# Performance work log

Measured on AMD Instinct MI355X. Metric: run time of the kernel, lower is better.

## Reference

```python
import jax, jax.numpy as jnp
import numpy as np
import math

B, S, D, H = 8, 1024, 256, 8
HD = D // H  # head size = 32


def setup_inputs() -> dict:
    key = jax.random.key(0)
    ks = jax.random.split(key, 12)
    inp = {
        "query": jax.random.normal(ks[0], (B, S, D), jnp.float32),
        "key": jax.random.normal(ks[1], (B, S, D), jnp.float32),
        "value": jax.random.normal(ks[2], (B, S, D), jnp.float32),
        "rel": jax.random.uniform(ks[3], (B, S, S), jnp.float32),
        "timestamp": jax.random.normal(ks[4], (B, S, S), jnp.float32),
        "l1": jax.random.uniform(ks[5], (1,), jnp.float32),
        "l2": jax.random.uniform(ks[6], (1,), jnp.float32),
        # projection weights (nn.Linear: y = x @ W.T + b)
        "Wq": jax.random.normal(ks[7], (D, D), jnp.float32) / math.sqrt(D),
        "bq": jnp.zeros((D,), jnp.float32),
        "Wk": jax.random.normal(ks[8], (D, D), jnp.float32) / math.sqrt(D),
        "bk": jnp.zeros((D,), jnp.float32),
        "Wv": jax.random.normal(ks[9], (D, D), jnp.float32) / math.sqrt(D),
        "bv": jnp.zeros((D,), jnp.float32),
    }
    return inp


def reference(query, key, value, rel, timestamp, l1, l2, Wq, bq, Wk, bk, Wv, bv):
    b, s, d = query.shape
    h, hd = H, HD

    def proj(x, W, bias):
        # [b,s,d] -> [b,h,s,hd]
        return (x @ W.T + bias).reshape(b, s, h, hd).transpose(0, 2, 1, 3)

    q = proj(query, Wq, bq)
    k = proj(key, Wk, bk)
    v = proj(value, Wv, bv)

    # causal future mask: True above the diagonal (future positions)
    mask = jnp.triu(jnp.ones((s, s), dtype=bool), k=1)[None, None]  # [1,1,s,s]

    # relation attention: rel * mask, zeros -> -10000, softmax
    relm = rel[:, None] * mask.astype(rel.dtype)  # broadcast over heads [b,1->h,s,s]
    rel_attn = jax.nn.softmax(jnp.where(relm == 0, jnp.float32(-10000.0), relm), axis=-1)

    # scaled dot-product scores with causal mask
    scores = jnp.einsum('bhqd,bhkd->bhqk', q, k) / math.sqrt(hd)
    scores = jnp.where(mask, jnp.float32(-1e9), scores)
    prob_attn = jax.nn.softmax(scores, axis=-1)

    # time-decay attention: exp(-|t|), masked to -inf (use -1e30 for grad safety)
    ts = jnp.where(mask, jnp.float32(-1e30), jnp.exp(-jnp.abs(timestamp[:, None])))
    time_attn = jax.nn.softmax(ts, axis=-1)

    # blend (time_include=True, qrelation_include=True)
    prob = (1.0 - l2) * prob_attn + l2 * time_attn
    prob = (1.0 - l1) * prob + l1 * rel_attn

    out = jnp.einsum('bhqk,bhkd->bhqd', prob, v)
    out = out.transpose(0, 2, 1, 3).reshape(b, s, d)
    return out
```

## Files before the change

### kernel.cpp

```cpp
#include <hip/hip_runtime.h>
#include <math.h>

constexpr int B = 8, S = 1024, D = 256, H = 8, HD = 32;

typedef __attribute__((ext_vector_type(8))) short bf16x8;
typedef __attribute__((ext_vector_type(16))) float f32x16;
typedef __attribute__((ext_vector_type(2)))  int  int2v;

__device__ __forceinline__ uint cvtpk(float a, float b) {
    uint r;
    asm("v_cvt_pk_bf16_f32 %0, %1, %2" : "=v"(r) : "v"(a), "v"(b));
    return r;
}
__device__ __forceinline__ float xswap32f(float v, int hi) {
    int2v t = __builtin_amdgcn_permlane32_swap(__float_as_int(v), __float_as_int(v), false, false);
    return __int_as_float(hi ? t[0] : t[1]);
}

__global__ __launch_bounds__(512, 4) void proj_mfma(
    const float* __restrict__ query, const float* __restrict__ key_,
    const float* __restrict__ value,
    const float* __restrict__ Wq, const float* __restrict__ Wk,
    const float* __restrict__ Wv,
    const float* __restrict__ bq, const float* __restrict__ bk,
    const float* __restrict__ bv, float qscale,
    ushort* __restrict__ qbuf, ushort* __restrict__ kbuf,
    ushort* __restrict__ vtbuf, float* __restrict__ cpart)
{
    __shared__ ushort xf[8192];
    __shared__ float bias_lds[256];

    const int m = blockIdx.y;
    const int tid = threadIdx.x;
    const int w = tid >> 6, lane = tid & 63;
    const int l31 = lane & 31, hi = lane >> 5;
    const int h = w;

    const float* xsrc = (m == 0) ? query : (m == 1) ? key_ : value;
    const float* Wsrc = (m == 0) ? Wq : (m == 1) ? Wk : Wv;
    const float* bsrc = (m == 0) ? bq : (m == 1) ? bk : bv;
    ushort* yb = (m == 0) ? qbuf : (m == 1) ? kbuf : vtbuf;
    const float wscale = (m == 0) ? qscale : 1.0f;

    if (tid < 256) bias_lds[tid] = bsrc[tid] * wscale;

    bf16x8 wf[16];
    {
        const float* wrow = Wsrc + ((size_t)(h * 32 + l31)) * 256 + hi * 8;
        #pragma unroll
        for (int kc = 0; kc < 16; ++kc) {
            float4 a = *(const float4*)(wrow + kc * 16);
            float4 b = *(const float4*)(wrow + kc * 16 + 4);
            uint4 p;
            p.x = cvtpk(a.x * wscale, a.y * wscale);
            p.y = cvtpk(a.z * wscale, a.w * wscale);
            p.z = cvtpk(b.x * wscale, b.y * wscale);
            p.w = cvtpk(b.z * wscale, b.w * wscale);
            wf[kc] = __builtin_bit_cast(bf16x8, p);
        }
    }

    const int sst = tid & 31, skc = tid >> 5;
    float cpacc = 0.f;

    for (int it = 0; it < 2; ++it) {
        const int stile = blockIdx.x * 2 + it;
        const int b_ = stile >> 5, t32 = stile & 31;

        __syncthreads();
        {
            const float* xrow = xsrc + ((size_t)(stile * 32 + sst)) * 256 + skc * 16;
            float4 a0 = *(const float4*)(xrow + 0);
            float4 a1 = *(const float4*)(xrow + 4);
            float4 a2 = *(const float4*)(xrow + 8);
            float4 a3 = *(const float4*)(xrow + 12);
            uint2 w01 = { cvtpk(a0.x, a0.y), cvtpk(a0.z, a0.w) };
            uint2 w23 = { cvtpk(a1.x, a1.y), cvtpk(a1.z, a1.w) };
            uint2 w45 = { cvtpk(a2.x, a2.y), cvtpk(a2.z, a2.w) };
            uint2 w67 = { cvtpk(a3.x, a3.y), cvtpk(a3.z, a3.w) };
            ushort* base = xf + skc * 512 + sst * 4;
            *(uint2*)(base +   0) = w01;
            *(uint2*)(base + 128) = w23;
            *(uint2*)(base + 256) = w45;
            *(uint2*)(base + 384) = w67;
        }
        __syncthreads();

        f32x16 acc;
        #pragma unroll
        for (int r = 0; r < 16; ++r) acc[r] = 0.f;
        #pragma unroll
        for (int kc = 0; kc < 16; ++kc) {
            const ushort* rb = xf + kc * 512 + hi * 256 + l31 * 4;
            uint2 lo = *(const uint2*)rb;
            uint2 hj = *(const uint2*)(rb + 128);
            uint4 xw = { lo.x, lo.y, hj.x, hj.y };
            bf16x8 xfrag = __builtin_bit_cast(bf16x8, xw);
            if (m < 2)
                acc = __builtin_amdgcn_mfma_f32_32x32x16_bf16(wf[kc], xfrag, acc, 0, 0, 0);
            else
                acc = __builtin_amdgcn_mfma_f32_32x32x16_bf16(xfrag, wf[kc], acc, 0, 0, 0);
        }

        if (m < 2) {
            #pragma unroll
            for (int r = 0; r < 16; ++r)
                acc[r] += bias_lds[h * 32 + (r & 3) + 8 * (r >> 2) + 4 * hi];
        } else {
            const float bl = bias_lds[h * 32 + l31];
            #pragma unroll
            for (int r = 0; r < 16; ++r) acc[r] += bl;
            float cp = 0.f;
            #pragma unroll
            for (int r = 0; r < 16; ++r) cp += acc[r];
            cp += __shfl_xor(cp, 32);
            cpacc += cp;
        }

        uint wa0 = cvtpk(acc[0], acc[1]),   wa1 = cvtpk(acc[2], acc[3]);
        uint wb0 = cvtpk(acc[4], acc[5]),   wb1 = cvtpk(acc[6], acc[7]);
        uint wa2 = cvtpk(acc[8], acc[9]),   wa3 = cvtpk(acc[10], acc[11]);
        uint wb2 = cvtpk(acc[12], acc[13]), wb3 = cvtpk(acc[14], acc[15]);
        int2v s0 = __builtin_amdgcn_permlane32_swap((int)wa0, (int)wb0, false, false);
        int2v s1 = __builtin_amdgcn_permlane32_swap((int)wa1, (int)wb1, false, false);
        int2v s2 = __builtin_amdgcn_permlane32_swap((int)wa2, (int)wb2, false, false);
        int2v s3 = __builtin_amdgcn_permlane32_swap((int)wa3, (int)wb3, false, false);
        uint4 p0 = { (uint)s0[0], (uint)s1[0], (uint)s0[1], (uint)s1[1] };
        uint4 p1 = { (uint)s2[0], (uint)s3[0], (uint)s2[1], (uint)s3[1] };
        ushort* dst = yb + (((size_t)b_ * H + h) * 32 + t32) * 1024 + hi * 256 + l31 * 8;
        *(uint4*)dst = p0;
        *(uint4*)(dst + 512) = p1;
    }
    if (m == 2 && hi == 0)
        cpart[blockIdx.x * D + h * 32 + l31] = cpacc;
}

__global__ __launch_bounds__(512, 2) void timerel_mfma(
    const float* __restrict__ ts, const float* __restrict__ rel,
    const ushort* __restrict__ vtb, const float* __restrict__ cpart,
    const float* __restrict__ l1p, const float* __restrict__ l2p,
    float* __restrict__ out)
{
    __shared__ ushort wlds[66 * 512];
    __shared__ float rsum[2][8][32];
    __shared__ float normt[32], normr[32], nuni[32];

    const int b  = blockIdx.y;
    const int i0 = blockIdx.x * 32;
    const int ksd = i0 >> 4;
    const int w = threadIdx.x >> 6, lane = threadIdx.x & 63;
    const int l31 = lane & 31, hi = lane >> 5;
    const int hi8 = hi * 8;
    const int i = i0 + l31;

    const float* tsrow  = ts  + ((size_t)b * S + i) * S + hi8;
    const float* relrow = rel + ((size_t)b * S + i) * S + hi8;

    float st = 0.f, sr = 0.f;
    const int ks0 = w * 8;
    #pragma unroll
    for (int kk = 0; kk < 8; ++kk) {
        const int ks = ks0 + kk;
        const int js = ks * 16;
        ushort* slotT = wlds + ks * 512 + hi * 256 + l31 * 4;
        if (ks < ksd) {
            float tv[8];
            *(float4*)&tv[0] = *(const float4*)(tsrow + js);
            *(float4*)&tv[4] = *(const float4*)(tsrow + js + 4);
            uint wp[4];
            #pragma unroll
            for (int q = 0; q < 4; ++q) {
                float w0 = __expf(__expf(-fabsf(tv[2 * q])));
                float w1 = __expf(__expf(-fabsf(tv[2 * q + 1])));
                st += w0 + w1;
                wp[q] = cvtpk(w0, w1);
            }
            uint2 v0; v0.x = wp[0]; v0.y = wp[1];
            uint2 v1; v1.x = wp[2]; v1.y = wp[3];
            *(uint2*)slotT         = v0;
            *(uint2*)(slotT + 128) = v1;
        } else if (ks > ksd + 1) {
            float rv[8];
            *(float4*)&rv[0] = *(const float4*)(relrow + js);
            *(float4*)&rv[4] = *(const float4*)(relrow + js + 4);
            uint wp[4];
            #pragma unroll
            for (int q = 0; q < 4; ++q) {
                float r0 = rv[2 * q], r1 = rv[2 * q + 1];
                float w0 = (r0 != 0.f) ? __expf(r0) : 0.f;
                float w1 = (r1 != 0.f) ? __expf(r1) : 0.f;
                sr += w0 + w1;
                wp[q] = cvtpk(w0, w1);
            }
            uint2 v0; v0.x = wp[0]; v0.y = wp[1];
            uint2 v1; v1.x = wp[2]; v1.y = wp[3];
            *(uint2*)slotT         = v0;
            *(uint2*)(slotT + 128) = v1;
        } else {
            float tv[8], rv[8];
            *(float4*)&tv[0] = *(const float4*)(tsrow + js);
            *(float4*)&tv[4] = *(const float4*)(tsrow + js + 4);
            *(float4*)&rv[0] = *(const float4*)(relrow + js);
            *(float4*)&rv[4] = *(const float4*)(relrow + js + 4);
            uint wpT[4], wpR[4];
            #pragma unroll
            for (int q = 0; q < 4; ++q) {
                const int j0 = js + hi8 + 2 * q;
                const bool p0 = (j0     <= i), p1 = (j0 + 1 <= i);
                float t0 = __expf(__expf(-fabsf(tv[2 * q])));
                float t1 = __expf(__expf(-fabsf(tv[2 * q + 1])));
                float r0 = (rv[2 * q]     != 0.f) ? __expf(rv[2 * q])     : 0.f;
                float r1 = (rv[2 * q + 1] != 0.f) ? __expf(rv[2 * q + 1]) : 0.f;
                float wT0 = p0 ? t0 : 0.f, wT1 = p1 ? t1 : 0.f;
                float wR0 = p0 ? 0.f : r0, wR1 = p1 ? 0.f : r1;
                st += wT0 + wT1; sr += wR0 + wR1;
                wpT[q] = cvtpk(wT0, wT1);
                wpR[q] = cvtpk(wR0, wR1);
            }
            uint2 t0v; t0v.x = wpT[0]; t0v.y = wpT[1];
            uint2 t1v; t1v.x = wpT[2]; t1v.y = wpT[3];
            *(uint2*)slotT         = t0v;
            *(uint2*)(slotT + 128) = t1v;
            ushort* slotR = wlds + (64 + (ks - ksd)) * 512 + hi * 256 + l31 * 4;
            uint2 r0v; r0v.x = wpR[0]; r0v.y = wpR[1];
            uint2 r1v; r1v.x = wpR[2]; r1v.y = wpR[3];
            *(uint2*)slotR         = r0v;
            *(uint2*)(slotR + 128) = r1v;
        }
    }

    st += __shfl_xor(st, 32);
    sr += __shfl_xor(sr, 32);
    if (hi == 0) { rsum[0][w][l31] = st; rsum[1][w][l31] = sr; }
    __syncthreads();

    if (threadIdx.x < 32) {
        const int r = threadIdx.x;
        float stt = 0.f, srt = 0.f;
        #pragma unroll
        for (int q = 0; q < 8; ++q) { stt += rsum[0][q][r]; srt += rsum[1][q][r]; }
        const float l1 = l1p[0], l2 = l2p[0];
        normt[r] = (1.f - l1) * l2 / stt;
        normr[r] = (srt > 0.5f) ? (l1 / srt) : 0.f;
        nuni[r]  = (srt > 0.5f) ? 0.f : (l1 / (float)S);
    }
    __syncthreads();

    const ushort* vtbase = vtb + ((size_t)b * 8 + w) * 32768 + hi * 256 + l31 * 8;
    f32x16 accT, accR;
    #pragma unroll
    for (int r = 0; r < 16; ++r) { accT[r] = 0.f; accR[r] = 0.f; }

    #define MSTEP(SLOT, VCH, ACC) do { \
        const ushort* rb = wlds + (SLOT) * 512 + hi * 256 + l31 * 4; \
        uint2 lo = *(const uint2*)rb; \
        uint2 hj = *(const uint2*)(rb + 128); \
        uint4 aw = { lo.x, lo.y, hj.x, hj.y }; \
        bf16x8 afrag = __builtin_bit_cast(bf16x8, aw); \
        bf16x8 vf = *(const bf16x8*)(vtbase + (size_t)(VCH) * 512); \
        ACC = __builtin_amdgcn_mfma_f32_32x32x16_bf16(afrag, vf, ACC, 0, 0, 0); \
    } while (0)

    const int nT = ksd + 2;
    #pragma unroll 4
    for (int ks = 0; ks < nT; ++ks) MSTEP(ks, ks, accT);
    MSTEP(64, ksd,     accR);
    MSTEP(65, ksd + 1, accR);
    #pragma unroll 4
    for (int ks = nT; ks < 64; ++ks) MSTEP(ks, ks, accR);
    #undef MSTEP

    const int d = w * 32 + l31;
    float cv = 0.f;
    if (i0 == S - 32) {
        #pragma unroll
        for (int p_ = 0; p_ < 16; ++p_)
            cv += cpart[(b * 16 + p_) * D + d];
    }
    float* obase = out + ((size_t)b * S + i0) * D + d;
    #pragma unroll
    for (int r = 0; r < 16; ++r) {
        const int row = (r & 3) + 8 * (r >> 2) + 4 * hi;
        obase[(size_t)row * D] =
            accT[r] * normt[row] + accR[r] * normr[row] + nuni[row] * cv;
    }
}

#define LOADKV(K0, K1, V0, V1, KT) do { \
    const ushort* kp_ = kbase + (size_t)(KT) * 1024; \
    const ushort* vp_ = vbase + (size_t)(KT) * 1024; \
    K0 = *(const bf16x8*)kp_;        K1 = *(const bf16x8*)(kp_ + 512); \
    V0 = *(const bf16x8*)vp_;        V1 = *(const bf16x8*)(vp_ + 512); \
} while (0)

#define TILE_COMPUTE(K0, K1, V0, V1, ISDIAG) do { \
    f32x16 stv; \
    _Pragma("unroll") for (int r = 0; r < 16; ++r) stv[r] = 0.f; \
    stv = __builtin_amdgcn_mfma_f32_32x32x16_bf16(K0, qf0, stv, 0, 0, 0); \
    stv = __builtin_amdgcn_mfma_f32_32x32x16_bf16(K1, qf1, stv, 0, 0, 0); \
    if (ISDIAG) { \
        _Pragma("unroll") for (int r = 0; r < 16; ++r) \
            if (((r & 3) + 8 * (r >> 2) + 4 * hi) > l31) stv[r] = -1e30f; \
    } \
    float p[16]; \
    _Pragma("unroll") for (int r = 0; r < 16; ++r) { p[r] = exp2f(stv[r]); lacc += p[r]; } \
    uint wa0 = cvtpk(p[0], p[1]),   wa1 = cvtpk(p[2], p[3]); \
    uint wb0 = cvtpk(p[4], p[5]),   wb1 = cvtpk(p[6], p[7]); \
    uint wa2 = cvtpk(p[8], p[9]),   wa3 = cvtpk(p[10], p[11]); \
    uint wb2 = cvtpk(p[12], p[13]), wb3 = cvtpk(p[14], p[15]); \
    int2v s0 = __builtin_amdgcn_permlane32_swap((int)wa0, (int)wb0, false, false); \
    int2v s1 = __builtin_amdgcn_permlane32_swap((int)wa1, (int)wb1, false, false); \
    int2v s2 = __builtin_amdgcn_permlane32_swap((int)wa2, (int)wb2, false, false); \
    int2v s3 = __builtin_amdgcn_permlane32_swap((int)wa3, (int)wb3, false, false); \
    uint4 pa0i = { (uint)s0[0], (uint)s1[0], (uint)s0[1], (uint)s1[1] }; \
    uint4 pa1i = { (uint)s2[0], (uint)s3[0], (uint)s2[1], (uint)s3[1] }; \
    bf16x8 pa0 = __builtin_bit_cast(bf16x8, pa0i); \
    bf16x8 pa1 = __builtin_bit_cast(bf16x8, pa1i); \
    ot = __builtin_amdgcn_mfma_f32_32x32x16_bf16(V0, pa0, ot, 0, 0, 0); \
    ot = __builtin_amdgcn_mfma_f32_32x32x16_bf16(V1, pa1, ot, 0, 0, 0); \
} while (0)

__global__ __launch_bounds__(512, 4) void flash_mfma(
    const ushort* __restrict__ qb, const ushort* __restrict__ kb,
    const ushort* __restrict__ vtb, const float* __restrict__ l1p,
    const float* __restrict__ l2p, float* __restrict__ out)
{
    __shared__ float mbuf[4][64][18];
    __shared__ float lds_t[4][32 * 33];
    const int id = blockIdx.x;
    const int halfg = id >> 8, rr_ = id & 255;
    const int qraw = rr_ >> 5;
    const int qblk = halfg ? (7 - qraw) : qraw;
    const int bh = (rr_ & 31) | (halfg << 5);
    const int b = bh >> 3, h = bh & 7;
    const int w = threadIdx.x >> 6, lane = threadIdx.x & 63;
    const int sub = w & 3, half = w >> 2;
    const int l31 = lane & 31, hi = lane >> 5;
    const int qt = qblk * 4 + sub;
    const float c_p = (1.f - l1p[0]) * (1.f - l2p[0]);

    const ushort* qp_ = qb + ((size_t)bh * 32 + qt) * 1024 + hi * 256 + l31 * 8;
    const bf16x8 qf0 = *(const bf16x8*)qp_;
    const bf16x8 qf1 = *(const bf16x8*)(qp_ + 512);
    const ushort* kbase = kb  + (size_t)bh * 32768 + hi * 256 + l31 * 8;
    const ushort* vbase = vtb + (size_t)bh * 32768 + hi * 256 + l31 * 8;

    f32x16 ot;
    #pragma unroll
    for (int r = 0; r < 16; ++r) ot[r] = 0.f;
    float lacc = 0.f;

    const int nlo = (qt + 1) >> 1;
    const int klo = half ? nlo : 0;
    const int khi = half ? qt : (nlo - 1);

    if (klo <= khi) {
        bf16x8 kA0, kA1, vA0, vA1, kB0, kB1, vB0, vB1;
        LOADKV(kA0, kA1, vA0, vA1, klo);
        int kt = klo;
        for (;;) {
            if (kt + 1 <= khi) LOADKV(kB0, kB1, vB0, vB1, kt + 1);
            TILE_COMPUTE(kA0, kA1, vA0, vA1, kt == qt);
            if (++kt > khi) break;
            if (kt + 1 <= khi) LOADKV(kA0, kA1, vA0, vA1, kt + 1);
            TILE_COMPUTE(kB0, kB1, vB0, vB1, kt == qt);
            if (++kt > khi) break;
        }
    }

    if (half == 1) {
        float* mb = &mbuf[sub][lane][0];
        #pragma unroll
        for (int r = 0; r < 16; r += 4)
            *(float4*)&mb[r] = make_float4(ot[r], ot[r+1], ot[r+2], ot[r+3]);
        mb[16] = lacc;
    }
    __syncthreads();

    if (half == 0) {
        const float* mb = &mbuf[sub][lane][0];
        #pragma unroll
        for (int r = 0; r < 16; ++r) ot[r] += mb[r];
        lacc += mb[16];
        const float lrun = lacc + xswap32f(lacc, hi);
        const float inv = c_p / lrun;
        float* lt = lds_t[sub];
        #pragma unroll
        for (int r = 0; r < 16; ++r) {
            const int d = (r & 3) + 8 * (r >> 2) + 4 * hi;
            lt[l31 * 33 + d] = ot[r] * inv;
        }
    }
    __syncthreads();
    if (half == 0) {
        const int q0w = qt * 32;
        const float* lt = lds_t[sub];
        #pragma unroll
        for (int rr = 0; rr < 4; ++rr) {
            const int ql = rr * 8 + (lane >> 3);
            const int d0 = (lane & 7) * 4;
            const float* lp = &lt[ql * 33 + d0];
            float* op = out + ((size_t)b * S + q0w + ql) * D + h * 32 + d0;
            float4 cur = *(const float4*)op;
            cur.x += lp[0]; cur.y += lp[1]; cur.z += lp[2]; cur.w += lp[3];
            *(float4*)op = cur;
        }
    }
}

extern "C" void kernel_launch(void* const* d_in, const int* in_sizes, int n_in,
                              void* d_out, int out_size, void* d_ws, size_t ws_size,
                              hipStream_t stream)
{
    (void)in_sizes; (void)n_in; (void)out_size; (void)ws_size;
    const float* query = (const float*)d_in[0];
    const float* key_  = (const float*)d_in[1];
    const float* value = (const float*)d_in[2];
    const float* rel   = (const float*)d_in[3];
    const float* tsp   = (const float*)d_in[4];
    const float* l1p   = (const float*)d_in[5];
    const float* l2p   = (const float*)d_in[6];
    const float* Wq    = (const float*)d_in[7];
    const float* bq    = (const float*)d_in[8];
    const float* Wk    = (const float*)d_in[9];
    const float* bk    = (const float*)d_in[10];
    const float* Wv    = (const float*)d_in[11];
    const float* bv    = (const float*)d_in[12];
    float* out = (float*)d_out;

    ushort* qbuf  = (ushort*)d_ws;
    ushort* kbuf  = (ushort*)((char*)d_ws + (4u  << 20));
    ushort* vtbuf = (ushort*)((char*)d_ws + (8u  << 20));
    float*  cpart = (float*)((char*)d_ws + (12u << 20));

    const float qscale = 1.4426950408889634f * 0.17677669529663687f;

    proj_mfma<<<dim3(128, 3), 512, 0, stream>>>(
        query, key_, value, Wq, Wk, Wv, bq, bk, bv, qscale,
        qbuf, kbuf, vtbuf, cpart);

    timerel_mfma<<<dim3(S / 32, B), 512, 0, stream>>>(
        tsp, rel, vtbuf, cpart, l1p, l2p, out);

    flash_mfma<<<512, 512, 0, stream>>>(qbuf, kbuf, vtbuf, l1p, l2p, out);
}
```

Baseline: 65.00 us.

## Split timerel MFMA reduction across two wave groups with LDS combine

Doubles the timerel_mfma block to 1024 threads. Each warp now handles half as many k-slices in the weight-building phase, and the MFMA loop over 66 slots is split between a lower and an upper group of 8 waves. The upper group writes its partial accumulators to a new LDS buffer, which the lower group adds before writing the output. The aim is more parallelism and latency hiding per block. The cost is extra LDS use, extra barriers, a runtime branch between the two accumulators inside the loop, and possibly lower occupancy from the larger shared-memory footprint.

```diff
diff --git a/kernel.cpp b/kernel.cpp
--- a/kernel.cpp
+++ b/kernel.cpp
@@ -135,14 +135,15 @@
         cpart[blockIdx.x * D + h * 32 + l31] = cpacc;
 }
 
-__global__ __launch_bounds__(512, 2) void timerel_mfma(
+__global__ __launch_bounds__(1024, 4) void timerel_mfma(
     const float* __restrict__ ts, const float* __restrict__ rel,
     const ushort* __restrict__ vtb, const float* __restrict__ cpart,
     const float* __restrict__ l1p, const float* __restrict__ l2p,
     float* __restrict__ out)
 {
     __shared__ ushort wlds[66 * 512];
-    __shared__ float rsum[2][8][32];
+    __shared__ float cbuf[8][64][17];
+    __shared__ float rsum[2][16][32];
     __shared__ float normt[32], normr[32], nuni[32];
 
     const int b  = blockIdx.y;
@@ -157,9 +158,9 @@
     const float* relrow = rel + ((size_t)b * S + i) * S + hi8;
 
     float st = 0.f, sr = 0.f;
-    const int ks0 = w * 8;
+    const int ks0 = w * 4;
     #pragma unroll
-    for (int kk = 0; kk < 8; ++kk) {
+    for (int kk = 0; kk < 4; ++kk) {
         const int ks = ks0 + kk;
         const int js = ks * 16;
         ushort* slotT = wlds + ks * 512 + hi * 256 + l31 * 4;
@@ -238,7 +239,7 @@
         const int r = threadIdx.x;
         float stt = 0.f, srt = 0.f;
         #pragma unroll
-        for (int q = 0; q < 8; ++q) { stt += rsum[0][q][r]; srt += rsum[1][q][r]; }
+        for (int q = 0; q < 16; ++q) { stt += rsum[0][q][r]; srt += rsum[1][q][r]; }
         const float l1 = l1p[0], l2 = l2p[0];
         normt[r] = (1.f - l1) * l2 / stt;
         normr[r] = (srt > 0.5f) ? (l1 / srt) : 0.f;
@@ -246,43 +247,54 @@
     }
     __syncthreads();
 
-    const ushort* vtbase = vtb + ((size_t)b * 8 + w) * 32768 + hi * 256 + l31 * 8;
+    const int wd = w & 7, upper = w >> 3;
+    const ushort* vtbase = vtb + ((size_t)b * 8 + wd) * 32768 + hi * 256 + l31 * 8;
     f32x16 accT, accR;
     #pragma unroll
     for (int r = 0; r < 16; ++r) { accT[r] = 0.f; accR[r] = 0.f; }
 
-    #define MSTEP(SLOT, VCH, ACC) do { \
-        const ushort* rb = wlds + (SLOT) * 512 + hi * 256 + l31 * 4; \
-        uint2 lo = *(const uint2*)rb; \
-        uint2 hj = *(const uint2*)(rb + 128); \
-        uint4 aw = { lo.x, lo.y, hj.x, hj.y }; \
-        bf16x8 afrag = __builtin_bit_cast(bf16x8, aw); \
-        bf16x8 vf = *(const bf16x8*)(vtbase + (size_t)(VCH) * 512); \
-        ACC = __builtin_amdgcn_mfma_f32_32x32x16_bf16(afrag, vf, ACC, 0, 0, 0); \
-    } while (0)
-
-    const int nT = ksd + 2;
-    #pragma unroll 4
-    for (int ks = 0; ks < nT; ++ks) MSTEP(ks, ks, accT);
-    MSTEP(64, ksd,     accR);
-    MSTEP(65, ksd + 1, accR);
-    #pragma unroll 4
-    for (int ks = nT; ks < 64; ++ks) MSTEP(ks, ks, accR);
-    #undef MSTEP
-
-    const int d = w * 32 + l31;
-    float cv = 0.f;
-    if (i0 == S - 32) {
-        #pragma unroll
-        for (int p_ = 0; p_ < 16; ++p_)
-            cv += cpart[(b * 16 + p_) * D + d];
-    }
-    float* obase = out + ((size_t)b * S + i0) * D + d;
-    #pragma unroll
-    for (int r = 0; r < 16; ++r) {
-        const int row = (r & 3) + 8 * (r >> 2) + 4 * hi;
-        obase[(size_t)row * D] =
-            accT[r] * normt[row] + accR[r] * normr[row] + nuni[row] * cv;
+    const int s_begin = upper ? 33 : 0;
+    const int s_end   = upper ? 66 : 33;
+    for (int s = s_begin; s < s_end; ++s) {
+        const int vch = (s < 64) ? s : (ksd + (s - 64));
+        const ushort* rb = wlds + s * 512 + hi * 256 + l31 * 4;
+        uint2 lo = *(const uint2*)rb;
+        uint2 hj = *(const uint2*)(rb + 128);
+        uint4 aw = { lo.x, lo.y, hj.x, hj.y };
+        bf16x8 afrag = __builtin_bit_cast(bf16x8, aw);
+        bf16x8 vf = *(const bf16x8*)(vtbase + (size_t)vch * 512);
+        const bool isT = (s < 64) && (s <= ksd + 1);
+        if (isT) accT = __builtin_amdgcn_mfma_f32_32x32x16_bf16(afrag, vf, accT, 0, 0, 0);
+        else     accR = __builtin_amdgcn_mfma_f32_32x32x16_bf16(afrag, vf, accR, 0, 0, 0);
+    }
+    __syncthreads();
+
+    if (upper) {
+        float* cb = &cbuf[wd][lane][0];
+        #pragma unroll
+        for (int r = 0; r < 16; ++r) {
+            const int row = (r & 3) + 8 * (r >> 2) + 4 * hi;
+            cb[r] = accT[r] * normt[row] + accR[r] * normr[row];
+        }
+    }
+    __syncthreads();
+
+    if (!upper) {
+        const int d = wd * 32 + l31;
+        float cv = 0.f;
+        if (i0 == S - 32) {
+            #pragma unroll
+            for (int p_ = 0; p_ < 16; ++p_)
+                cv += cpart[(b * 16 + p_) * D + d];
+        }
+        const float* cb = &cbuf[wd][lane][0];
+        float* obase = out + ((size_t)b * S + i0) * D + d;
+        #pragma unroll
+        for (int r = 0; r < 16; ++r) {
+            const int row = (r & 3) + 8 * (r >> 2) + 4 * hi;
+            obase[(size_t)row * D] =
+                accT[r] * normt[row] + accR[r] * normr[row] + cb[r] + nuni[row] * cv;
+        }
     }
 }
 
@@ -439,7 +451,7 @@
         query, key_, value, Wq, Wk, Wv, bq, bk, bv, qscale,
         qbuf, kbuf, vtbuf, cpart);
 
-    timerel_mfma<<<dim3(S / 32, B), 512, 0, stream>>>(
+    timerel_mfma<<<dim3(S / 32, B), 1024, 0, stream>>>(
         tsp, rel, vtbuf, cpart, l1p, l2p, out);
 
     flash_mfma<<<512, 512, 0, stream>>>(qbuf, kbuf, vtbuf, l1p, l2p, out);
```

New measurement: 66.84 us. 2.8% more time.
